# Performance work log

Measured on AMD Instinct MI355X. Metric: run time of the kernel, lower is better.

Reference implementation:

```python
import jax, jax.numpy as jnp
import numpy as np


def setup_inputs() -> dict:
    key = jax.random.key(0)
    ks = jax.random.split(key, 5)
    B, M, R = 32, 32, 128
    d_lang, d_region, d_rank, d_fusion = 1024, 2048, 256, 256
    u = jax.random.normal(ks[0], (B, M, d_lang), dtype=jnp.float32)
    v = jax.random.normal(ks[1], (B, R, d_region), dtype=jnp.float32)
    # Linear weights stored torch-style as (out_features, in_features)
    Wu = jax.random.normal(ks[2], (d_rank, d_lang), dtype=jnp.float32) * (1.0 / np.sqrt(d_lang))
    Wv = jax.random.normal(ks[3], (d_rank, d_region), dtype=jnp.float32) * (1.0 / np.sqrt(d_region))
    Wp = jax.random.normal(ks[4], (d_fusion, d_rank), dtype=jnp.float32) * (1.0 / np.sqrt(d_rank))
    bp = jnp.zeros((d_fusion,), dtype=jnp.float32)
    return {"u": u, "v": v, "Wu": Wu, "Wv": Wv, "Wp": Wp, "bp": bp}


def reference(u, v, Wu, Wv, Wp, bp):
    # u: (B, M, d_lang), v: (B, R, d_region)
    up = jnp.einsum('bmd,rd->bmr', u, Wu)          # (B, M, d_rank)  [rd: out x in]
    vp = jnp.einsum('bnd,rd->bnr', v, Wv)          # (B, R, d_rank)
    # broadcast bilinear multiply: (B, M, R, d_rank)
    prod = up[:, :, None, :] * vp[:, None, :, :]
    o = jnp.einsum('bmnk,fk->bmnf', prod, Wp) + bp  # p-linear -> (B, M, R, d_fusion)
    # dropout is identity in inference mode
    return jax.nn.relu(o)
```

## Files before the change

### kernel.cpp

```cpp
#include <hip/hip_runtime.h>
#include <hip/hip_bf16.h>


typedef __attribute__((ext_vector_type(8))) short short8;
typedef __attribute__((ext_vector_type(4))) float floatx4;
typedef __attribute__((ext_vector_type(4))) unsigned uintx4;

__device__ __forceinline__ short f2bf(float f) {
    union { float f; unsigned u; } cv; cv.f = f;
    unsigned r = cv.u + 0x7fffu + ((cv.u >> 16) & 1u);
    return (short)(r >> 16);
}
__device__ __forceinline__ unsigned pack_rne(float x, float y) {
    __hip_bfloat162 h = __float22bfloat162_rn(make_float2(x, y));
    union { __hip_bfloat162 h; unsigned u; } cv; cv.h = h;
    return cv.u;
}

#define GL2LDS(gptr, lptr) __builtin_amdgcn_global_load_lds(                    \
    (const __attribute__((address_space(1))) void*)(gptr),                      \
    (__attribute__((address_space(3))) void*)(lptr), 16, 0, 0)

#define MFMA16(a, b, c) __builtin_amdgcn_mfma_f32_16x16x32_bf16((a), (b), (c), 0, 0, 0)

__global__ __launch_bounds__(256) void proj_kernel(
    const float* __restrict__ u, const float* __restrict__ Wu,
    float* __restrict__ upf,
    const float* __restrict__ v, const float* __restrict__ Wv,
    short* __restrict__ vpb)
{
    __shared__ __align__(16) short Xs[2][32 * 64];
    __shared__ __align__(16) short Wsh[2][64 * 64];

    const int tid  = threadIdx.x;
    const int lane = tid & 63;
    const int wave = tid >> 6;
    const int quad = lane >> 4;
    const int l15  = lane & 15;

    const int bid = blockIdx.x;
    const int xcd = bid & 7, j = bid >> 3;
    const int cb  = j & 3;
    const int pidx = xcd + 8 * (j >> 2);
    const float *X, *W; int D, r0; bool is_u;
    if (pidx < 32) { is_u = true;  X = u; W = Wu; D = 1024; r0 = pidx * 32; }
    else           { is_u = false; X = v; W = Wv; D = 2048; r0 = (pidx - 32) * 32; }
    const int c0 = cb * 64;
    const int wr = (wave >> 1) * 16;
    const int wc = (wave & 1) * 32;

    const int xr_ = tid >> 3, xk = (tid & 7) * 8;
    const int wr_ = tid >> 2, wk = (tid & 3) * 16;
    const float* xg = X + (size_t)(r0 + xr_) * D + xk;
    const float* wg = W + (size_t)(c0 + wr_) * D + wk;
    const int xswz  = (xr_ & 7) << 4;
    const int wswz  = (wr_ & 7) << 4;
    const int xbase = xr_ * 128 + xk * 2;
    const int wbase = wr_ * 128 + wk * 2;

    floatx4 acc[2] = {};
    float4 x0, x1, y0, y1, y2, y3;

#define LDC(k)                                                                  \
    x0 = *(const float4*)(xg + (k));      x1 = *(const float4*)(xg + (k) + 4);  \
    y0 = *(const float4*)(wg + (k));      y1 = *(const float4*)(wg + (k) + 4);  \
    y2 = *(const float4*)(wg + (k) + 8);  y3 = *(const float4*)(wg + (k) + 12);

#define PKC(bi)                                                                 \
    { char* xb = (char*)&Xs[bi][0]; char* wb = (char*)&Wsh[bi][0]; uintx4 q;    \
      q[0] = pack_rne(x0.x, x0.y); q[1] = pack_rne(x0.z, x0.w);                 \
      q[2] = pack_rne(x1.x, x1.y); q[3] = pack_rne(x1.z, x1.w);                 \
      *(uintx4*)(xb + (xbase ^ xswz)) = q;                                      \
      q[0] = pack_rne(y0.x, y0.y); q[1] = pack_rne(y0.z, y0.w);                 \
      q[2] = pack_rne(y1.x, y1.y); q[3] = pack_rne(y1.z, y1.w);                 \
      *(uintx4*)(wb + (wbase ^ wswz)) = q;                                      \
      q[0] = pack_rne(y2.x, y2.y); q[1] = pack_rne(y2.z, y2.w);                 \
      q[2] = pack_rne(y3.x, y3.y); q[3] = pack_rne(y3.z, y3.w);                 \
      *(uintx4*)(wb + ((wbase + 16) ^ wswz)) = q; }

    LDC(0); PKC(0);
    __syncthreads();

    const int asw = (l15 & 7) << 4;
    int cur = 0;
    for (int kc = 0; kc < D; kc += 64) {
        const bool has = (kc + 64) < D;
        if (has) { LDC(kc + 64); }

        const char* xb = (const char*)&Xs[cur][0];
        const char* wb = (const char*)&Wsh[cur][0];
        short8 a0  = *(const short8*)(xb + (((wr + l15) * 128 +      quad * 16) ^ asw));
        short8 a1  = *(const short8*)(xb + (((wr + l15) * 128 + 64 + quad * 16) ^ asw));
        short8 b00 = *(const short8*)(wb + (((wc +      l15) * 128 +      quad * 16) ^ asw));
        short8 b01 = *(const short8*)(wb + (((wc +      l15) * 128 + 64 + quad * 16) ^ asw));
        short8 b10 = *(const short8*)(wb + (((wc + 16 + l15) * 128 +      quad * 16) ^ asw));
        short8 b11 = *(const short8*)(wb + (((wc + 16 + l15) * 128 + 64 + quad * 16) ^ asw));
        acc[0] = MFMA16(a0, b00, acc[0]);
        acc[1] = MFMA16(a0, b10, acc[1]);
        acc[0] = MFMA16(a1, b01, acc[0]);
        acc[1] = MFMA16(a1, b11, acc[1]);

        if (has) { PKC(cur ^ 1); }
        __syncthreads();
        cur ^= 1;
    }
#undef LDC
#undef PKC

    if (is_u) {
#pragma unroll
        for (int tf = 0; tf < 2; tf++)
#pragma unroll
            for (int r = 0; r < 4; r++) {
                const int row = r0 + wr + quad * 4 + r;
                const int col = c0 + wc + tf * 16 + l15;
                upf[(size_t)row * 256 + col] = acc[tf][r];
            }
    } else {
#pragma unroll
        for (int tf = 0; tf < 2; tf++)
#pragma unroll
            for (int r = 0; r < 4; r++) {
                const int row = r0 + wr + quad * 4 + r;
                const int col = c0 + wc + tf * 16 + l15;
                vpb[(size_t)row * 256 + col] = f2bf(acc[tf][r]);
            }
    }
}

__global__ __launch_bounds__(256) void bilinear_kernel(
    const float* __restrict__ up, const short* __restrict__ vp,
    const float* __restrict__ Wp, const float* __restrict__ bp,
    float* __restrict__ out)
{
    __shared__ __align__(16) short vp_s[2][128 * 32];
    __shared__ __align__(16) float up_s[256];

    const int tid  = threadIdx.x;
    const int lane = tid & 63;
    const int wave = tid >> 6;
    const int quad = lane >> 4;
    const int l15  = lane & 15;

    const int bid = blockIdx.x;
    const int xcd = bid & 7;
    const int grp = bid >> 3;
    const int s   = grp & 63;
    const int b   = (grp >> 6) * 8 + xcd;
    const int m   = s >> 1;
    const int f_blk = s & 1;
    const int bm  = b * 32 + m;
    const int f0  = f_blk * 128;
    const int wn  = (wave >> 1) * 64;
    const int wf  = (wave & 1) * 64;

    const int sr = tid >> 2, q = tid & 3;
    const int qg = q ^ ((sr >> 1) & 3);
    const short* vg0 = vp + (size_t)(b * 128 +      sr) * 256 + qg * 8;
    const short* vg1 = vp + (size_t)(b * 128 + 64 + sr) * 256 + qg * 8;

    up_s[tid] = up[(size_t)bm * 256 + tid];

    const float* wpg = Wp + (size_t)(f0 + wf + l15) * 256 + quad * 8;

    GL2LDS(vg0, &vp_s[0][sr * 32 + q * 8]);
    GL2LDS(vg1, &vp_s[0][(64 + sr) * 32 + q * 8]);
    float4 w[4][2];
#pragma unroll
    for (int tt = 0; tt < 4; tt++) {
        w[tt][0] = *(const float4*)(wpg + tt * 4096);
        w[tt][1] = *(const float4*)(wpg + tt * 4096 + 4);
    }
    __syncthreads();

    floatx4 acc[4][4] = {};
    const int aslot = (quad ^ ((l15 >> 1) & 3)) * 16;

#pragma unroll
    for (int kc = 0; kc < 256; kc += 32) {
        const int cur = (kc >> 5) & 1;
        const int nxt = cur ^ 1;
        const bool has = kc < 224;

        if (has) {
            GL2LDS(vg0 + kc + 32, &vp_s[nxt][sr * 32 + q * 8]);
            GL2LDS(vg1 + kc + 32, &vp_s[nxt][(64 + sr) * 32 + q * 8]);
        }

        const float4 ua = *(const float4*)&up_s[kc + quad * 8];
        const float4 ub = *(const float4*)&up_s[kc + quad * 8 + 4];
        short8 bb[4];
#pragma unroll
        for (int tt = 0; tt < 4; tt++) {
            uintx4 o;
            o[0] = pack_rne(w[tt][0].x * ua.x, w[tt][0].y * ua.y);
            o[1] = pack_rne(w[tt][0].z * ua.z, w[tt][0].w * ua.w);
            o[2] = pack_rne(w[tt][1].x * ub.x, w[tt][1].y * ub.y);
            o[3] = pack_rne(w[tt][1].z * ub.z, w[tt][1].w * ub.w);
            union { uintx4 u; short8 s; } cv; cv.u = o;
            bb[tt] = cv.s;
        }

        float4 wnx[4][2];
        if (has) {
#pragma unroll
            for (int tt = 0; tt < 4; tt++) {
                wnx[tt][0] = *(const float4*)(wpg + tt * 4096 + kc + 32);
                wnx[tt][1] = *(const float4*)(wpg + tt * 4096 + kc + 36);
            }
        }

        short8 a[4];
#pragma unroll
        for (int tt = 0; tt < 4; tt++) {
            const int row = wn + tt * 16 + l15;
            a[tt] = *(const short8*)((const char*)&vp_s[cur][0] + row * 64 + aslot);
        }

#pragma unroll
        for (int tn = 0; tn < 4; tn++)
#pragma unroll
            for (int tf = 0; tf < 4; tf++)
                acc[tn][tf] = MFMA16(a[tn], bb[tf], acc[tn][tf]);

        if (has) {
#pragma unroll
            for (int tt = 0; tt < 4; tt++) { w[tt][0] = wnx[tt][0]; w[tt][1] = wnx[tt][1]; }
        }
        __syncthreads();
    }

    float bpv[4];
#pragma unroll
    for (int tf = 0; tf < 4; tf++) bpv[tf] = bp[f0 + wf + tf * 16 + l15];

    const size_t out_base = (size_t)bm * 128 * 256;
#pragma unroll
    for (int tn = 0; tn < 4; tn++)
#pragma unroll
        for (int r = 0; r < 4; r++) {
            const int n = wn + tn * 16 + quad * 4 + r;
            float* op = out + out_base + (size_t)n * 256 + f0 + wf + l15;
#pragma unroll
            for (int tf = 0; tf < 4; tf++) {
                float val = acc[tn][tf][r] + bpv[tf];
                op[tf * 16] = fmaxf(val, 0.0f);
            }
        }
}

extern "C" void kernel_launch(void* const* d_in, const int* in_sizes, int n_in,
                              void* d_out, int out_size, void* d_ws, size_t ws_size,
                              hipStream_t stream) {
    const float* u  = (const float*)d_in[0];
    const float* v  = (const float*)d_in[1];
    const float* Wu = (const float*)d_in[2];
    const float* Wv = (const float*)d_in[3];
    const float* Wp = (const float*)d_in[4];
    const float* bp = (const float*)d_in[5];
    float* out = (float*)d_out;

    float* up_f  = (float*)d_ws;
    short* vp_bf = (short*)(up_f + 262144);

    proj_kernel<<<dim3(640), dim3(256), 0, stream>>>(
        u, Wu, up_f, v, Wv, vp_bf);
    bilinear_kernel<<<dim3(2048), dim3(256), 0, stream>>>(
        up_f, vp_bf, Wp, bp, out);
}
```

Baseline: 250.7 us.

## Scale vp rows by u in LDS and pre-convert Wp to bf16

Moves the per-m scaling by up from the Wp operand onto the vp operand. Each block prescales its full 128x256 vp tile into swizzled LDS once, instead of converting and multiplying fp32 Wp every k-step. Wp is converted to bf16 once in the projection kernel and streamed directly as the MFMA B operand. This removes the per-iteration barriers and packing work from the main loop. The cost is a much larger LDS footprint (64KB), which limits occupancy, plus an extra prologue phase.

New measurement: 238.8 us. -4.8%, faster.

```diff
diff --git a/kernel.cpp b/kernel.cpp
--- a/kernel.cpp
+++ b/kernel.cpp
@@ -16,10 +16,11 @@
     union { __hip_bfloat162 h; unsigned u; } cv; cv.h = h;
     return cv.u;
 }
-
-#define GL2LDS(gptr, lptr) __builtin_amdgcn_global_load_lds(                    \
-    (const __attribute__((address_space(1))) void*)(gptr),                      \
-    (__attribute__((address_space(3))) void*)(lptr), 16, 0, 0)
+__device__ __forceinline__ unsigned scale2_rne(short a, short b, float ua, float ub) {
+    float x = __uint_as_float(((unsigned)(unsigned short)a) << 16) * ua;
+    float y = __uint_as_float(((unsigned)(unsigned short)b) << 16) * ub;
+    return pack_rne(x, y);
+}
 
 #define MFMA16(a, b, c) __builtin_amdgcn_mfma_f32_16x16x32_bf16((a), (b), (c), 0, 0, 0)
 
@@ -27,7 +28,8 @@
     const float* __restrict__ u, const float* __restrict__ Wu,
     float* __restrict__ upf,
     const float* __restrict__ v, const float* __restrict__ Wv,
-    short* __restrict__ vpb)
+    short* __restrict__ vpb,
+    const float* __restrict__ Wp, short* __restrict__ Wp_bf)
 {
     __shared__ __align__(16) short Xs[2][32 * 64];
     __shared__ __align__(16) short Wsh[2][64 * 64];
@@ -39,6 +41,17 @@
     const int l15  = lane & 15;
 
     const int bid = blockIdx.x;
+
+    if (bid < 32) {
+        const int widx = (bid * 256 + tid) * 8;
+        float4 g0 = *(const float4*)(Wp + widx);
+        float4 g1 = *(const float4*)(Wp + widx + 4);
+        short8 o;
+        o[0] = f2bf(g0.x); o[1] = f2bf(g0.y); o[2] = f2bf(g0.z); o[3] = f2bf(g0.w);
+        o[4] = f2bf(g1.x); o[5] = f2bf(g1.y); o[6] = f2bf(g1.z); o[7] = f2bf(g1.w);
+        *(short8*)(Wp_bf + widx) = o;
+    }
+
     const int xcd = bid & 7, j = bid >> 3;
     const int cb  = j & 3;
     const int pidx = xcd + 8 * (j >> 2);
@@ -130,11 +143,11 @@
 
 __global__ __launch_bounds__(256) void bilinear_kernel(
     const float* __restrict__ up, const short* __restrict__ vp,
-    const float* __restrict__ Wp, const float* __restrict__ bp,
+    const short* __restrict__ Wp_bf, const float* __restrict__ bp,
     float* __restrict__ out)
 {
-    __shared__ __align__(16) short vp_s[2][128 * 32];
-    __shared__ __align__(16) float up_s[256];
+    __shared__ __align__(16) short A_lds[128 * 256];
+    __shared__ float up_s[256];
 
     const int tid  = threadIdx.x;
     const int lane = tid & 63;
@@ -154,80 +167,68 @@
     const int wn  = (wave >> 1) * 64;
     const int wf  = (wave & 1) * 64;
 
-    const int sr = tid >> 2, q = tid & 3;
-    const int qg = q ^ ((sr >> 1) & 3);
-    const short* vg0 = vp + (size_t)(b * 128 +      sr) * 256 + qg * 8;
-    const short* vg1 = vp + (size_t)(b * 128 + 64 + sr) * 256 + qg * 8;
-
     up_s[tid] = up[(size_t)bm * 256 + tid];
-
-    const float* wpg = Wp + (size_t)(f0 + wf + l15) * 256 + quad * 8;
-
-    GL2LDS(vg0, &vp_s[0][sr * 32 + q * 8]);
-    GL2LDS(vg1, &vp_s[0][(64 + sr) * 32 + q * 8]);
-    float4 w[4][2];
-#pragma unroll
-    for (int tt = 0; tt < 4; tt++) {
-        w[tt][0] = *(const float4*)(wpg + tt * 4096);
-        w[tt][1] = *(const float4*)(wpg + tt * 4096 + 4);
-    }
     __syncthreads();
 
+    {
+        const int jrow = (tid >> 2) * 2;
+        const int kseg = (tid & 3) * 64;
+        const short* vsrc = vp + (size_t)(b * 128 + jrow) * 256 + kseg;
+        char* Ab = (char*)A_lds;
+#pragma unroll
+        for (int i = 0; i < 8; i++) {
+            const float4 ua = *(const float4*)&up_s[kseg + i * 8];
+            const float4 ub = *(const float4*)&up_s[kseg + i * 8 + 4];
+#pragma unroll
+            for (int r = 0; r < 2; r++) {
+                short8 vv = *(const short8*)(vsrc + r * 256 + i * 8);
+                uintx4 o;
+                o[0] = scale2_rne(vv[0], vv[1], ua.x, ua.y);
+                o[1] = scale2_rne(vv[2], vv[3], ua.z, ua.w);
+                o[2] = scale2_rne(vv[4], vv[5], ub.x, ub.y);
+                o[3] = scale2_rne(vv[6], vv[7], ub.z, ub.w);
+                const int row = jrow + r;
+                const int byte = (row * 512 + (kseg + i * 8) * 2) ^ ((row & 7) << 4);
+                *(uintx4*)(Ab + byte) = o;
+            }
+        }
+    }
+    __syncthreads();
+
     floatx4 acc[4][4] = {};
-    const int aslot = (quad ^ ((l15 >> 1) & 3)) * 16;
+    const char* Ab = (const char*)A_lds;
+    const int aswz = (l15 & 7) << 4;
+    const short* wq = Wp_bf + (size_t)(f0 + wf + l15) * 256 + quad * 8;
+
+    short8 bcur[4], bnxt[4];
+#pragma unroll
+    for (int tt = 0; tt < 4; tt++)
+        bcur[tt] = *(const short8*)(wq + tt * 4096);
 
 #pragma unroll
     for (int kc = 0; kc < 256; kc += 32) {
-        const int cur = (kc >> 5) & 1;
-        const int nxt = cur ^ 1;
-        const bool has = kc < 224;
-
-        if (has) {
-            GL2LDS(vg0 + kc + 32, &vp_s[nxt][sr * 32 + q * 8]);
-            GL2LDS(vg1 + kc + 32, &vp_s[nxt][(64 + sr) * 32 + q * 8]);
-        }
-
-        const float4 ua = *(const float4*)&up_s[kc + quad * 8];
-        const float4 ub = *(const float4*)&up_s[kc + quad * 8 + 4];
-        short8 bb[4];
-#pragma unroll
-        for (int tt = 0; tt < 4; tt++) {
-            uintx4 o;
-            o[0] = pack_rne(w[tt][0].x * ua.x, w[tt][0].y * ua.y);
-            o[1] = pack_rne(w[tt][0].z * ua.z, w[tt][0].w * ua.w);
-            o[2] = pack_rne(w[tt][1].x * ub.x, w[tt][1].y * ub.y);
-            o[3] = pack_rne(w[tt][1].z * ub.z, w[tt][1].w * ub.w);
-            union { uintx4 u; short8 s; } cv; cv.u = o;
-            bb[tt] = cv.s;
-        }
-
-        float4 wnx[4][2];
-        if (has) {
-#pragma unroll
-            for (int tt = 0; tt < 4; tt++) {
-                wnx[tt][0] = *(const float4*)(wpg + tt * 4096 + kc + 32);
-                wnx[tt][1] = *(const float4*)(wpg + tt * 4096 + kc + 36);
-            }
-        }
-
+        if (kc < 224) {
+#pragma unroll
+            for (int tt = 0; tt < 4; tt++)
+                bnxt[tt] = *(const short8*)(wq + tt * 4096 + kc + 32);
+        }
         short8 a[4];
 #pragma unroll
         for (int tt = 0; tt < 4; tt++) {
             const int row = wn + tt * 16 + l15;
-            a[tt] = *(const short8*)((const char*)&vp_s[cur][0] + row * 64 + aslot);
-        }
-
+            a[tt] = *(const short8*)(Ab + ((row * 512 + kc * 2 + quad * 16) ^ aswz));
+        }
+        __builtin_amdgcn_s_setprio(1);
 #pragma unroll
         for (int tn = 0; tn < 4; tn++)
 #pragma unroll
             for (int tf = 0; tf < 4; tf++)
-                acc[tn][tf] = MFMA16(a[tn], bb[tf], acc[tn][tf]);
-
-        if (has) {
-#pragma unroll
-            for (int tt = 0; tt < 4; tt++) { w[tt][0] = wnx[tt][0]; w[tt][1] = wnx[tt][1]; }
-        }
-        __syncthreads();
+                acc[tn][tf] = MFMA16(a[tn], bcur[tf], acc[tn][tf]);
+        __builtin_amdgcn_s_setprio(0);
+        if (kc < 224) {
+#pragma unroll
+            for (int tt = 0; tt < 4; tt++) bcur[tt] = bnxt[tt];
+        }
     }
 
     float bpv[4];
@@ -262,9 +263,10 @@
 
     float* up_f  = (float*)d_ws;
     short* vp_bf = (short*)(up_f + 262144);
+    short* Wp_bf = vp_bf + 1048576;
 
     proj_kernel<<<dim3(640), dim3(256), 0, stream>>>(
-        u, Wu, up_f, v, Wv, vp_bf);
+        u, Wu, up_f, v, Wv, vp_bf, Wp, Wp_bf);
     bilinear_kernel<<<dim3(2048), dim3(256), 0, stream>>>(
-        up_f, vp_bf, Wp, bp, out);
-}
+        up_f, vp_bf, Wp_bf, bp, out);
+}
```
